# Optimization experiments

Hardware: AMD Instinct MI355X
Metric: run time of the kernel (lower is better)

Reference implementation:

```python
import jax, jax.numpy as jnp
import numpy as np

H = 16   # num_attention_heads
G = 4    # num_gqa_groups
D = 64   # head_dim = hidden // H
HIDDEN = 1024
KV_DIM = HIDDEN // H * G  # 256
EPS = 1e-5


def setup_inputs() -> dict:
    key = jax.random.key(0)
    k0, k1, k2, k3 = jax.random.split(key, 4)
    x = jax.random.normal(k0, (8, 4096, HIDDEN), dtype=jnp.float32)
    query_weight = jax.random.normal(k1, (HIDDEN, HIDDEN), dtype=jnp.float32) * 0.02
    key_weight = jax.random.normal(k2, (KV_DIM, HIDDEN), dtype=jnp.float32) * 0.02
    value_weight = jax.random.normal(k3, (KV_DIM, HIDDEN), dtype=jnp.float32) * 0.02
    return {
        "x": x,
        "query_weight": query_weight,
        "key_weight": key_weight,
        "value_weight": value_weight,
        "query_bias": jnp.zeros((HIDDEN,), jnp.float32),
        "key_bias": jnp.zeros((KV_DIM,), jnp.float32),
        "value_bias": jnp.zeros((KV_DIM,), jnp.float32),
        "layer_norm_weight": jnp.ones((HIDDEN,), jnp.float32),
        "layer_norm_bias": jnp.zeros((HIDDEN,), jnp.float32),
    }


def reference(x, query_weight, key_weight, value_weight, query_bias, key_bias,
              value_bias, layer_norm_weight, layer_norm_bias):
    b, s, _ = x.shape
    # Shared LayerNorm (q is k is v path in apply_qkv_norm)
    mu = jnp.mean(x, axis=-1, keepdims=True)
    var = jnp.mean(jnp.square(x - mu), axis=-1, keepdims=True)
    xn = (x - mu) * jax.lax.rsqrt(var + EPS) * layer_norm_weight + layer_norm_bias
    # Q/K/V projections (F.linear: x @ W.T + b)
    q = xn @ query_weight.T + query_bias           # [b, s, H*D]
    k = xn @ key_weight.T + key_bias               # [b, s, G*1*D]
    v = xn @ value_weight.T + value_bias           # [b, s, G*1*D]
    # 'b s (h d) -> b h s d'
    q = q.reshape(b, s, H, D).transpose(0, 2, 1, 3)           # [b, H, s, D]
    # 'b s (g h d) -> b h (g s) d' with h = KV_DIM//(G*D) = 1
    def kv_rearrange(t):
        t = t.reshape(b, s, G, 1, D)                          # b s g h d
        t = t.transpose(0, 3, 2, 1, 4)                        # b h g s d
        return t.reshape(b, 1, G * s, D)                      # [b, 1, G*s, D]
    return q, kv_rearrange(k), kv_rearrange(v)
```

## Files before the change

kernel.cpp:

```cpp
#include <hip/hip_runtime.h>
#include <hip/hip_bf16.h>


#define HIDDEN 1024
#define NTOK   32768

typedef __bf16 bf16x8 __attribute__((ext_vector_type(8)));
typedef float  f32x4  __attribute__((ext_vector_type(4)));

#define GLOBAL_AS(p) ((const __attribute__((address_space(1))) void*)(p))
#define LDS_AS(p)    ((__attribute__((address_space(3))) void*)(p))

__device__ __forceinline__ unsigned short f2bf(float f) {
  union { float f; unsigned int i; } x; x.f = f;
  unsigned int r = x.i + 0x7FFFu + ((x.i >> 16) & 1u);
  return (unsigned short)(r >> 16);
}

__global__ __launch_bounds__(256) void ln_kernel(
    const float* __restrict__ x,
    const float* __restrict__ gamma,
    const float* __restrict__ beta,
    unsigned short* __restrict__ xn) {
  const int row = blockIdx.x;
  const int t   = threadIdx.x;
  const size_t base = (size_t)row * HIDDEN;

  const float4 v = ((const float4*)(x + base))[t];
  float s  = v.x + v.y + v.z + v.w;
  float s2 = v.x*v.x + v.y*v.y + v.z*v.z + v.w*v.w;
#pragma unroll
  for (int off = 32; off >= 1; off >>= 1) {
    s  += __shfl_xor(s,  off);
    s2 += __shfl_xor(s2, off);
  }
  __shared__ float red[8];
  const int w = t >> 6;
  if ((t & 63) == 0) { red[w] = s; red[4 + w] = s2; }
  __syncthreads();
  s  = red[0] + red[1] + red[2] + red[3];
  s2 = red[4] + red[5] + red[6] + red[7];
  const float mu   = s * (1.0f / HIDDEN);
  const float rstd = rsqrtf(s2 * (1.0f / HIDDEN) - mu * mu + 1e-5f);

  const float4 g  = ((const float4*)gamma)[t];
  const float4 bb = ((const float4*)beta)[t];
  ushort4 o;
  o.x = f2bf((v.x - mu) * rstd * g.x + bb.x);
  o.y = f2bf((v.y - mu) * rstd * g.y + bb.y);
  o.z = f2bf((v.z - mu) * rstd * g.z + bb.z);
  o.w = f2bf((v.w - mu) * rstd * g.w + bb.w);
  ((ushort4*)(xn + base))[t] = o;
}

__global__ __launch_bounds__(256) void cvt_kernel(
    const float* __restrict__ src, unsigned short* __restrict__ dst) {
  const int i = blockIdx.x * 256 + threadIdx.x;
  const float4 v = ((const float4*)src)[i];
  ushort4 o;
  o.x = f2bf(v.x); o.y = f2bf(v.y); o.z = f2bf(v.z); o.w = f2bf(v.w);
  ((ushort4*)dst)[i] = o;
}

__global__ __launch_bounds__(512, 2) void qkv_gemm(
    const unsigned short* __restrict__ xn,
    const unsigned short* __restrict__ wq,
    const unsigned short* __restrict__ wk,
    const unsigned short* __restrict__ wv,
    const float* __restrict__ bq,
    const float* __restrict__ bk,
    const float* __restrict__ bv,
    float* __restrict__ out) {
  __shared__ unsigned short Alds[32768];
  __shared__ unsigned short Blds[32768];

  const int bid = blockIdx.x;
  const int swz = (bid & 7) * 96 + (bid >> 3);
  const int mt  = swz / 6;
  const int nt  = swz % 6;
  const int brow = mt * 256;

  const unsigned short* wbase; const float* biasptr;
  int segcol; size_t obase; int hg;
  if (nt < 4)       { wbase = wq + (size_t)nt * 256 * HIDDEN; biasptr = bq; segcol = nt * 256; obase = 0u;        hg = 16; }
  else if (nt == 4) { wbase = wk;                             biasptr = bk; segcol = 0;        obase = 33554432u; hg = 4;  }
  else              { wbase = wv;                             biasptr = bv; segcol = 0;        obase = 41943040u; hg = 4;  }

  const int t = threadIdx.x;
  const int w = t >> 6, lane = t & 63;
  const int wm = w >> 2, wn = w & 3;
  const int l15 = lane & 15, hi = lane >> 4;

  const int sr  = 2 * w * 16 + (lane >> 2);
  const int scg = ((lane & 3) ^ ((lane >> 2) & 3)) * 8;
  const unsigned short* aST = xn    + (size_t)(brow + sr) * HIDDEN + scg;
  const unsigned short* bST = wbase + (size_t)sr * HIDDEN + scg;
  const int ldsq = 2 * w * 512;

  const int rdx  = (hi ^ (l15 & 3)) * 8;
  const int rowA = wm * 128 + l15;
  const int rowB = wn * 64  + l15;

  f32x4 acc[8][4];
#pragma unroll
  for (int m = 0; m < 8; ++m)
#pragma unroll
    for (int n = 0; n < 4; ++n) acc[m][n] = (f32x4){0.f, 0.f, 0.f, 0.f};
  bf16x8 a[8], b[2];

#define STA(BUF, KK, KT) do {                                                   \
    unsigned short* _d = Alds + (BUF) * 16384 + (KK) * 8192 + ldsq;             \
    const unsigned short* _s = aST + (size_t)((KT) * 64 + (KK) * 32);           \
    __builtin_amdgcn_global_load_lds(GLOBAL_AS(_s), LDS_AS(_d), 16, 0, 0);      \
    __builtin_amdgcn_global_load_lds(GLOBAL_AS(_s + 16 * HIDDEN), LDS_AS(_d + 512), 16, 0, 0); \
  } while (0)
#define STB(BUF, KK, KT) do {                                                   \
    unsigned short* _d = Blds + (BUF) * 16384 + (KK) * 8192 + ldsq;             \
    const unsigned short* _s = bST + (size_t)((KT) * 64 + (KK) * 32);           \
    __builtin_amdgcn_global_load_lds(GLOBAL_AS(_s), LDS_AS(_d), 16, 0, 0);      \
    __builtin_amdgcn_global_load_lds(GLOBAL_AS(_s + 16 * HIDDEN), LDS_AS(_d + 512), 16, 0, 0); \
  } while (0)
#define DSA(BUF, KK) do { _Pragma("unroll")                                     \
    for (int m = 0; m < 8; ++m)                                                 \
      a[m] = *(const bf16x8*)(Alds + (BUF) * 16384 + (KK) * 8192 + (rowA + m * 16) * 32 + rdx); \
  } while (0)
#define DSB(BUF, KK, NB) do { _Pragma("unroll")                                 \
    for (int n = 0; n < 2; ++n)                                                 \
      b[n] = *(const bf16x8*)(Blds + (BUF) * 16384 + (KK) * 8192 + (rowB + ((NB) + n) * 16) * 32 + rdx); \
  } while (0)
#define MM(NB) do {                                                             \
    __builtin_amdgcn_s_setprio(1);                                              \
    _Pragma("unroll") for (int m = 0; m < 8; ++m) {                             \
      acc[m][(NB)]     = __builtin_amdgcn_mfma_f32_16x16x32_bf16(a[m], b[0], acc[m][(NB)], 0, 0, 0);     \
      acc[m][(NB) + 1] = __builtin_amdgcn_mfma_f32_16x16x32_bf16(a[m], b[1], acc[m][(NB) + 1], 0, 0, 0); \
    }                                                                           \
    __builtin_amdgcn_s_setprio(0);                                              \
  } while (0)
#define BARS do { __builtin_amdgcn_s_barrier();                                 \
    asm volatile("s_waitcnt lgkmcnt(0)" ::: "memory");                          \
    __builtin_amdgcn_sched_barrier(0); } while (0)
#define ENDB do { __builtin_amdgcn_s_barrier();                                 \
    __builtin_amdgcn_sched_barrier(0); } while (0)
#define VMW(N) asm volatile("s_waitcnt vmcnt(" #N ")" ::: "memory")

  STA(0, 0, 0); STB(0, 0, 0); STA(0, 1, 0); STB(0, 1, 0);
  STA(1, 0, 1); STB(1, 0, 1); STA(1, 1, 1);
  VMW(10);
  __builtin_amdgcn_s_barrier();
  __builtin_amdgcn_sched_barrier(0);

  for (int i = 0; i < 7; ++i) {
    const int T = 2 * i;
     DSA(0, 0); DSB(0, 0, 0); STB(1, 1, T + 1); BARS; MM(0);          ENDB;
     DSB(0, 0, 2);            STA(0, 0, T + 2); BARS; MM(2); VMW(10); ENDB;
     DSA(0, 1); DSB(0, 1, 0); STB(0, 0, T + 2); BARS; MM(0);          ENDB;
     DSB(0, 1, 2);            STA(0, 1, T + 2); BARS; MM(2); VMW(10); ENDB;
     DSA(1, 0); DSB(1, 0, 0); STB(0, 1, T + 2); BARS; MM(0);          ENDB;
     DSB(1, 0, 2);            STA(1, 0, T + 3); BARS; MM(2); VMW(10); ENDB;
     DSA(1, 1); DSB(1, 1, 0); STB(1, 0, T + 3); BARS; MM(0);          ENDB;
     DSB(1, 1, 2);            STA(1, 1, T + 3); BARS; MM(2); VMW(10); ENDB;
  }
   DSA(0, 0); DSB(0, 0, 0); STB(1, 1, 15); BARS; MM(0);         ENDB;
   DSB(0, 0, 2);                           BARS; MM(2); VMW(8); ENDB;
   DSA(0, 1); DSB(0, 1, 0);                BARS; MM(0);         ENDB;
   DSB(0, 1, 2);                           BARS; MM(2); VMW(4); ENDB;
   DSA(1, 0); DSB(1, 0, 0);                BARS; MM(0);         ENDB;
   DSB(1, 0, 2);                           BARS; MM(2); VMW(0); ENDB;
   DSA(1, 1); DSB(1, 1, 0);                BARS; MM(0);         ENDB;
   DSB(1, 1, 2);                           BARS; MM(2);         ENDB;

#undef STA
#undef STB
#undef DSA
#undef DSB
#undef MM
#undef BARS
#undef ENDB
#undef VMW

  const int col_l = l15;
  const int row_l = hi * 4;
#pragma unroll
  for (int n = 0; n < 4; ++n) {
    const int ncolseg = segcol + wn * 64 + n * 16 + col_l;
    const float bias = biasptr[ncolseg];
    const int g = ncolseg >> 6;
    const int d = ncolseg & 63;
#pragma unroll
    for (int m = 0; m < 8; ++m) {
#pragma unroll
      for (int j = 0; j < 4; ++j) {
        const int token = brow + wm * 128 + m * 16 + row_l + j;
        const int b_ = token >> 12, s = token & 4095;
        const size_t off = obase + (size_t)(b_ * hg + g) * 262144u + (size_t)s * 64u + d;
        out[off] = acc[m][n][j] + bias;
      }
    }
  }
}

extern "C" void kernel_launch(void* const* d_in, const int* in_sizes, int n_in,
                              void* d_out, int out_size, void* d_ws, size_t ws_size,
                              hipStream_t stream) {
  const float* x  = (const float*)d_in[0];
  const float* wq = (const float*)d_in[1];
  const float* wk = (const float*)d_in[2];
  const float* wv = (const float*)d_in[3];
  const float* bq = (const float*)d_in[4];
  const float* bk = (const float*)d_in[5];
  const float* bv = (const float*)d_in[6];
  const float* g  = (const float*)d_in[7];
  const float* be = (const float*)d_in[8];
  float* out = (float*)d_out;

  unsigned short* xn  = (unsigned short*)d_ws;
  unsigned short* wqb = (unsigned short*)((char*)d_ws + (64u << 20));
  unsigned short* wkb = wqb + 1024 * 1024;
  unsigned short* wvb = wkb + 256 * 1024;

  ln_kernel<<<NTOK, 256, 0, stream>>>(x, g, be, xn);
  cvt_kernel<<<1024, 256, 0, stream>>>(wq, wqb);
  cvt_kernel<<<256,  256, 0, stream>>>(wk, wkb);
  cvt_kernel<<<256,  256, 0, stream>>>(wv, wvb);
  qkv_gemm<<<768, 512, 0, stream>>>(xn, wqb, wkb, wvb, bq, bk, bv, out);
}
```

Before: 188.1 us.

## Stage GEMM epilogue through LDS for coalesced float4 stores; retune LDS swizzle

Replaces the scattered per-element fp32 output stores with a per-wave LDS staging pass. Each wave writes its 16x64 accumulator slice into padded LDS and reads it back as float4 rows, so global writes become contiguous 256-byte head rows. It also changes the XOR swizzle used for the A/B LDS tiles, with matching read indices, to cut bank conflicts. The cost is an extra LDS round trip that reuses the A buffer after the main loop, relying on wave-local ordering without a block barrier.

```diff
diff --git a/kernel.cpp b/kernel.cpp
--- a/kernel.cpp
+++ b/kernel.cpp
@@ -92,12 +92,12 @@
   const int l15 = lane & 15, hi = lane >> 4;
 
   const int sr  = 2 * w * 16 + (lane >> 2);
-  const int scg = ((lane & 3) ^ ((lane >> 2) & 3)) * 8;
+  const int scg = ((lane & 3) ^ ((lane >> 3) & 3)) * 8;
   const unsigned short* aST = xn    + (size_t)(brow + sr) * HIDDEN + scg;
   const unsigned short* bST = wbase + (size_t)sr * HIDDEN + scg;
   const int ldsq = 2 * w * 512;
 
-  const int rdx  = (hi ^ (l15 & 3)) * 8;
+  const int rdx  = (hi ^ ((l15 >> 1) & 3)) * 8;
   const int rowA = wm * 128 + l15;
   const int rowB = wn * 64  + l15;
 
@@ -178,23 +178,31 @@
 #undef ENDB
 #undef VMW
 
-  const int col_l = l15;
-  const int row_l = hi * 4;
-#pragma unroll
-  for (int n = 0; n < 4; ++n) {
-    const int ncolseg = segcol + wn * 64 + n * 16 + col_l;
-    const float bias = biasptr[ncolseg];
-    const int g = ncolseg >> 6;
-    const int d = ncolseg & 63;
-#pragma unroll
-    for (int m = 0; m < 8; ++m) {
-#pragma unroll
-      for (int j = 0; j < 4; ++j) {
-        const int token = brow + wm * 128 + m * 16 + row_l + j;
-        const int b_ = token >> 12, s = token & 4095;
-        const size_t off = obase + (size_t)(b_ * hg + g) * 262144u + (size_t)s * 64u + d;
-        out[off] = acc[m][n][j] + bias;
-      }
+  float* ep = (float*)Alds;
+  const int epb = w * 1344;
+  const int headcol = segcol + wn * 64;
+  const int gidx = headcol >> 6;
+  const int tok0 = brow + wm * 128;
+  const int b_ = tok0 >> 12;
+  float* wout = out + obase + (size_t)(b_ * hg + gidx) * 262144u
+                    + (size_t)(tok0 & 4095) * 64u;
+  float biasv[4];
+#pragma unroll
+  for (int n = 0; n < 4; ++n) biasv[n] = biasptr[headcol + n * 16 + l15];
+
+#pragma unroll
+  for (int m = 0; m < 8; ++m) {
+#pragma unroll
+    for (int n = 0; n < 4; ++n)
+#pragma unroll
+      for (int j = 0; j < 4; ++j)
+        ep[epb + (hi * 4 + j) * 84 + n * 16 + l15] = acc[m][n][j] + biasv[n];
+    asm volatile("s_waitcnt lgkmcnt(0)" ::: "memory");
+#pragma unroll
+    for (int it = 0; it < 4; ++it) {
+      const int r = it * 4 + hi;
+      const float4 v = *(const float4*)(ep + epb + r * 84 + l15 * 4);
+      *(float4*)(wout + (size_t)(m * 16 + r) * 64 + l15 * 4) = v;
     }
   }
 }
```

Measured after the change: 176.5 us. -6.2%, faster.
